# Performance work log

Measured on AMD Instinct MI355X. Metric: run time of the kernel, lower is better.

## Reference

```python
import jax, jax.numpy as jnp
import numpy as np

B, T, D = 4096, 200, 64
H1, H2 = 128, 64


def setup_inputs() -> dict:
    key = jax.random.key(0)
    ks = jax.random.split(key, 9)
    def glorot(k, shape):
        fan_in, fan_out = shape[0], shape[1]
        lim = float(np.sqrt(6.0 / (fan_in + fan_out)))
        return jax.random.uniform(k, shape, jnp.float32, -lim, lim)
    return {
        "candidate_embedding": jax.random.normal(ks[0], (B, D), jnp.float32),
        "history_embeddings": jax.random.normal(ks[1], (B, T, D), jnp.float32),
        "mask": jax.random.randint(ks[2], (B, T), 0, 2, jnp.int32),
        "W1": glorot(ks[3], (4 * D, H1)),
        "b1": jnp.zeros((H1,), jnp.float32),
        "W2": glorot(ks[4], (H1, H2)),
        "b2": jnp.zeros((H2,), jnp.float32),
        "W3": glorot(ks[5], (H2, 1)),
        "b3": jnp.zeros((1,), jnp.float32),
    }


def reference(candidate_embedding, history_embeddings, mask, W1, b1, W2, b2, W3, b3):
    # candidate: [B, D] -> broadcast to [B, T, D]
    cand = candidate_embedding[:, None, :]  # [B, 1, D]
    cand = jnp.broadcast_to(cand, history_embeddings.shape)
    # DIN feature concat: [B, T, 4D]
    feats = jnp.concatenate(
        [cand, history_embeddings, cand - history_embeddings, cand * history_embeddings],
        axis=-1,
    )
    # small MLP scorer per position
    h = jax.nn.relu(jnp.einsum("btf,fh->bth", feats, W1) + b1)
    h = jax.nn.relu(jnp.einsum("btf,fh->bth", h, W2) + b2)
    scores = (jnp.einsum("btf,fo->bto", h, W3) + b3)[..., 0]  # [B, T]
    # masked softmax over T
    scores = jnp.where(mask == 0, jnp.float32(-1e9), scores)
    weights = jax.nn.softmax(scores, axis=1)  # [B, T]
    # weighted sum over history: [B, D]
    return jnp.einsum("btd,bt->bd", history_embeddings, weights)
```

## Files before the change

### kernel.cpp

```cpp
#include <hip/hip_runtime.h>
#include <hip/hip_bf16.h>

#define NB 4096
#define NT 200
#define ND 64
#define NH1 128
#define NH2 64

#define WS_WX 0
#define WS_WC 16384
#define WS_W2 24576
#define WS_B1 32768
#define WS_B2 32896
#define WS_W3 32960
#define WS_B3 33024

__device__ __align__(16) float  g_wxt[8192];
__device__ __align__(16) float  g_wdt[8192];
__device__ __align__(16) __bf16 g_w2ts[8192];
__device__ __align__(16) __bf16 g_w2tsh[8192];
__device__ __align__(16) __bf16 g_w2tsl[8192];

typedef __bf16 bf16x8 __attribute__((ext_vector_type(8)));
typedef __bf16 bf16x4 __attribute__((ext_vector_type(4)));
typedef float  f32x4  __attribute__((ext_vector_type(4)));

__device__ __forceinline__ float ldany(const void* p, int i, int bf) {
    if (bf) return __bfloat162float(((const __hip_bfloat16*)p)[i]);
    return ((const float*)p)[i];
}

__global__ __launch_bounds__(256) void prep_kernel(
    const void* W1, const void* b1, const void* W2, const void* b2,
    const void* W3, const void* b3, int* flag_out, float* F) {
    __shared__ int votes;
    int tid = threadIdx.x;
    if (tid == 0) votes = 0;
    __syncthreads();
    {
        const unsigned* w1u = (const unsigned*)W1;
        unsigned w = w1u[tid];
        unsigned lo = w & 0xFFFFu;
        unsigned e = (lo >> 7) & 0xFFu;
        if (lo == 0u || (e >= 96u && e <= 124u)) atomicAdd(&votes, 1);
    }
    __syncthreads();
    int bf = (votes >= 160) ? 1 : 0;
    if (blockIdx.x == 0 && tid == 0) flag_out[0] = bf;

    int gtid = blockIdx.x * blockDim.x + tid;
    int gstride = gridDim.x * blockDim.x;

    for (int e = gtid; e < 8192; e += gstride) {
        int k = e >> 7, j = e & 127;
        float w1b = ldany(W1, (64 + k) * 128 + j, bf);
        float w1c = ldany(W1, (128 + k) * 128 + j, bf);
        float w1a = ldany(W1, k * 128 + j, bf);
        float w1d = ldany(W1, (192 + k) * 128 + j, bf);
        float wx = w1b - w1c;
        F[WS_WX + e] = wx;
        F[WS_WX + 8192 + e] = w1d;
        F[WS_WC + e] = w1a + w1c;
        g_wxt[j * 64 + k] = wx;
        g_wdt[j * 64 + k] = w1d;
        float w2v = ldany(W2, e, bf);
        F[WS_W2 + e] = w2v;
        int j2 = e & 63, k2 = e >> 6;
        int so = j2 * 128 + (k2 ^ ((j2 & 15) << 3));
        g_w2ts[so] = (__bf16)w2v;
        __bf16 w2h = (__bf16)w2v;
        g_w2tsh[so] = w2h;
        g_w2tsl[so] = (__bf16)(w2v - (float)w2h);
    }
    for (int e = gtid; e < 128; e += gstride) F[WS_B1 + e] = ldany(b1, e, bf);
    for (int e = gtid; e < 64; e += gstride) {
        F[WS_B2 + e] = ldany(b2, e, bf);
        F[WS_W3 + e] = ldany(W3, e, bf);
    }
    if (gtid == 0) F[WS_B3] = ldany(b3, 0, bf);
}

__device__ __forceinline__ void compute_chunk(
    int w, int lane, int tbase, int b, const int* mask,
    const __bf16* sH, const __bf16* sWhi, const __bf16* sWlo,
    const __bf16* sW2, __bf16* h1hi, __bf16* h1lo,
    const float* cbias, const float* b2s, const float* W3s, float b3v,
    float* ss)
{
    const int lq = lane >> 4, lr = lane & 15;
    const int t0 = 16 * w;

    const int ar = t0 + lr;
    const int asw = (ar & 7) << 3;
    const bf16x8 a0 = *(const bf16x8*)&sH[ar * 64 + ((lq * 8) ^ asw)];
    const bf16x8 a1 = *(const bf16x8*)&sH[ar * 64 + ((32 + lq * 8) ^ asw)];

#pragma unroll
    for (int n = 0; n < 8; n++) {
        const int col = n * 16 + lr;
        const int bsw = (col & 7) << 3;
        const int wb = col * 64;
        const float cb = cbias[col];
        f32x4 c = {cb, cb, cb, cb};
        c = __builtin_amdgcn_mfma_f32_16x16x32_bf16(
                a0, *(const bf16x8*)&sWhi[wb + ((lq * 8) ^ bsw)], c, 0, 0, 0);
        c = __builtin_amdgcn_mfma_f32_16x16x32_bf16(
                a1, *(const bf16x8*)&sWhi[wb + ((32 + lq * 8) ^ bsw)], c, 0, 0, 0);
        c = __builtin_amdgcn_mfma_f32_16x16x32_bf16(
                a0, *(const bf16x8*)&sWlo[wb + ((lq * 8) ^ bsw)], c, 0, 0, 0);
        c = __builtin_amdgcn_mfma_f32_16x16x32_bf16(
                a1, *(const bf16x8*)&sWlo[wb + ((32 + lq * 8) ^ bsw)], c, 0, 0, 0);
#pragma unroll
        for (int r = 0; r < 4; r++) {
            const int row = lq * 4 + r;
            const int hoff = row * 128 + (col ^ ((row & 15) << 3));
            float v = fmaxf(c[r], 0.f);
            __bf16 hi = (__bf16)v;
            h1hi[hoff] = hi;
            h1lo[hoff] = (__bf16)(v - (float)hi);
        }
    }

    f32x4 acc2[4];
#pragma unroll
    for (int n = 0; n < 4; n++) {
        const float bb = b2s[n * 16 + lr];
        acc2[n] = (f32x4){bb, bb, bb, bb};
    }
    const int a2sw = lr << 3;
#pragma unroll
    for (int s = 0; s < 4; s++) {
        const int k0 = s * 32 + lq * 8;
        const bf16x8 ah = *(const bf16x8*)&h1hi[lr * 128 + (k0 ^ a2sw)];
        const bf16x8 al = *(const bf16x8*)&h1lo[lr * 128 + (k0 ^ a2sw)];
#pragma unroll
        for (int n = 0; n < 4; n++) {
            const int col = n * 16 + lr;
            const bf16x8 bb =
                *(const bf16x8*)&sW2[col * 128 + (k0 ^ ((col & 15) << 3))];
            acc2[n] = __builtin_amdgcn_mfma_f32_16x16x32_bf16(ah, bb, acc2[n], 0, 0, 0);
            acc2[n] = __builtin_amdgcn_mfma_f32_16x16x32_bf16(al, bb, acc2[n], 0, 0, 0);
        }
    }

#pragma unroll
    for (int r = 0; r < 4; r++) {
        float p = 0.f;
#pragma unroll
        for (int n = 0; n < 4; n++)
            p = fmaf(fmaxf(acc2[n][r], 0.f), W3s[n * 16 + lr], p);
        p += __shfl_xor(p, 1);
        p += __shfl_xor(p, 2);
        p += __shfl_xor(p, 4);
        p += __shfl_xor(p, 8);
        const int gt = tbase + t0 + lq * 4 + r;
        if (lr == 0 && gt < NT)
            ss[gt] = (mask[(long)b * NT + gt] != 0) ? (p + b3v) : -1e9f;
    }
}

__global__ __launch_bounds__(512) void attn_bf16_kernel(
    const void* cand, const void* hist, const int* mask,
    const int* flag_p, const float* F, void* out)
{
    if (flag_p[0] == 0) return;

    __shared__ __align__(16) __bf16 sWhi[8192];
    __shared__ __align__(16) __bf16 sWlo[8192];
    __shared__ __align__(16) __bf16 sW2[8192];
    __shared__ __align__(16) __bf16 sH[8192];
    __shared__ __align__(16) __bf16 sH1[32768];
    __shared__ float cbias[128];
    __shared__ float cs[64], W3s[64], b2s[64];
    __shared__ float ss[NT];
    __shared__ float sred[8];
    __shared__ float part[8 * 65];
    __shared__ float b3s;

    const int tid = threadIdx.x;
    const int b = blockIdx.x;
    const int w = tid >> 6, lane = tid & 63;
    const __hip_bfloat16* hp = (const __hip_bfloat16*)hist;

    if (tid < 64) {
        cs[tid] = __bfloat162float(((const __hip_bfloat16*)cand)[(long)b * 64 + tid]);
        W3s[tid] = F[WS_W3 + tid];
        b2s[tid] = F[WS_B2 + tid];
    }
    if (tid == 0) b3s = F[WS_B3];
    *(uint4*)((char*)sW2 + tid * 16) =
        *(const uint4*)((const char*)g_w2ts + tid * 16);
    *(uint4*)((char*)sW2 + 8192 + tid * 16) =
        *(const uint4*)((const char*)g_w2ts + 8192 + tid * 16);
#pragma unroll
    for (int i = 0; i < 2; i++) {
        const int idx = tid + i * 512;
        const int t = idx >> 3, q = idx & 7;
        uint4 v = *(const uint4*)(hp + ((long)b * NT + t) * 64 + q * 8);
        *(uint4*)&sH[t * 64 + ((q * 8) ^ ((t & 7) << 3))] = v;
    }
    __syncthreads();

#pragma unroll
    for (int i = 0; i < 16; i++) {
        const int e = tid + i * 512;
        const int j = e >> 6, k = e & 63;
        float wv = fmaf(cs[k], g_wdt[e], g_wxt[e]);
        __bf16 hi = (__bf16)wv;
        const int off = j * 64 + (k ^ ((j & 7) << 3));
        sWhi[off] = hi;
        sWlo[off] = (__bf16)(wv - (float)hi);
    }
    {
        const int j = tid >> 2, kq = (tid & 3) << 4;
        float a = 0.f;
#pragma unroll
        for (int k2 = 0; k2 < 16; k2++)
            a = fmaf(cs[kq + k2], F[WS_WC + (kq + k2) * 128 + j], a);
        a += __shfl_xor(a, 1);
        a += __shfl_xor(a, 2);
        if ((tid & 3) == 0) cbias[j] = a + F[WS_B1 + j];
    }
    uint4 c1a, c1b = {0, 0, 0, 0};
    {
        const int t = 128 + (tid >> 3), q = tid & 7;
        c1a = *(const uint4*)(hp + ((long)b * NT + t) * 64 + q * 8);
    }
    if (tid < 64) {
        const int t = 192 + (tid >> 3), q = tid & 7;
        c1b = *(const uint4*)(hp + ((long)b * NT + t) * 64 + q * 8);
    }
    __builtin_amdgcn_sched_barrier(0);
    __syncthreads();

    const float b3v = b3s;
    compute_chunk(w, lane, 0, b, mask, sH, sWhi, sWlo, sW2,
                  &sH1[w * 4096], &sH1[w * 4096 + 2048],
                  cbias, b2s, W3s, b3v, ss);
    __syncthreads();

    {
        const int t = tid >> 3, q = tid & 7;
        *(uint4*)&sH[t * 64 + ((q * 8) ^ ((t & 7) << 3))] = c1a;
    }
    if (tid < 64) {
        const int t = 64 + (tid >> 3), q = tid & 7;
        *(uint4*)&sH[t * 64 + ((q * 8) ^ ((t & 7) << 3))] = c1b;
    }
    if (tid < 64) {
        const int t = 72 + (tid >> 3), q = tid & 7;
        uint4 z = {0, 0, 0, 0};
        *(uint4*)&sH[t * 64 + ((q * 8) ^ ((t & 7) << 3))] = z;
    }
    __syncthreads();

    if (w < 5)
        compute_chunk(w, lane, 128, b, mask, sH, sWhi, sWlo, sW2,
                      &sH1[w * 4096], &sH1[w * 4096 + 2048],
                      cbias, b2s, W3s, b3v, ss);
    __syncthreads();

    float v = (tid < NT) ? ss[tid] : -3.0e38f;
    if (tid < 256) {
        float m = v;
#pragma unroll
        for (int o = 32; o; o >>= 1) m = fmaxf(m, __shfl_xor(m, o));
        if ((tid & 63) == 0) sred[tid >> 6] = m;
    }
    __syncthreads();
    const float M = fmaxf(fmaxf(sred[0], sred[1]), fmaxf(sred[2], sred[3]));
    float p = (tid < NT) ? __expf(v - M) : 0.f;
    if (tid < 256) {
        float s2 = p;
#pragma unroll
        for (int o = 32; o; o >>= 1) s2 += __shfl_xor(s2, o);
        if ((tid & 63) == 0) sred[4 + (tid >> 6)] = s2;
    }
    __syncthreads();
    const float S = sred[4] + sred[5] + sred[6] + sred[7];
    if (tid < NT) ss[tid] = p / S;
    __syncthreads();

    const int d = tid & 63, g = tid >> 6;
    float acc = 0.f;
    for (int t = g; t < NT; t += 8)
        acc = fmaf(ss[t], __bfloat162float(hp[((long)b * NT + t) * 64 + d]), acc);
    part[g * 65 + d] = acc;
    __syncthreads();
    if (tid < 64) {
        float o = 0.f;
#pragma unroll
        for (int g2 = 0; g2 < 8; g2++) o += part[g2 * 65 + tid];
        ((__hip_bfloat16*)out)[b * 64 + tid] = __float2bfloat16(o);
    }
}

__device__ __forceinline__ void compute_chunk_f32(
    int w, int lane, int tbase, int b, const int* mask,
    const __bf16* sHhi, const __bf16* sHlo,
    const __bf16* sWhi, const __bf16* sWlo,
    const __bf16* sW2h, const __bf16* sW2l,
    __bf16* h1hi, __bf16* h1lo,
    const float* cbias, const float* b2s, const float* W3s, float b3v,
    float* ss)
{
    const int lq = lane >> 4, lr = lane & 15;
    const int t0 = 16 * w;

    const int ar = t0 + lr;
    const int asw = (ar & 7) << 3;
    const bf16x8 a0h = *(const bf16x8*)&sHhi[ar * 64 + ((lq * 8) ^ asw)];
    const bf16x8 a1h = *(const bf16x8*)&sHhi[ar * 64 + ((32 + lq * 8) ^ asw)];
    const bf16x8 a0l = *(const bf16x8*)&sHlo[ar * 64 + ((lq * 8) ^ asw)];
    const bf16x8 a1l = *(const bf16x8*)&sHlo[ar * 64 + ((32 + lq * 8) ^ asw)];
    __syncthreads();

#pragma unroll
    for (int n = 0; n < 8; n++) {
        const int col = n * 16 + lr;
        const int bsw = (col & 7) << 3;
        const int wb = col * 64;
        const float cb = cbias[col];
        f32x4 c = {cb, cb, cb, cb};
        const bf16x8 bh0 = *(const bf16x8*)&sWhi[wb + ((lq * 8) ^ bsw)];
        const bf16x8 bh1 = *(const bf16x8*)&sWhi[wb + ((32 + lq * 8) ^ bsw)];
        const bf16x8 bl0 = *(const bf16x8*)&sWlo[wb + ((lq * 8) ^ bsw)];
        const bf16x8 bl1 = *(const bf16x8*)&sWlo[wb + ((32 + lq * 8) ^ bsw)];
        c = __builtin_amdgcn_mfma_f32_16x16x32_bf16(a0h, bh0, c, 0, 0, 0);
        c = __builtin_amdgcn_mfma_f32_16x16x32_bf16(a1h, bh1, c, 0, 0, 0);
        c = __builtin_amdgcn_mfma_f32_16x16x32_bf16(a0l, bh0, c, 0, 0, 0);
        c = __builtin_amdgcn_mfma_f32_16x16x32_bf16(a1l, bh1, c, 0, 0, 0);
        c = __builtin_amdgcn_mfma_f32_16x16x32_bf16(a0h, bl0, c, 0, 0, 0);
        c = __builtin_amdgcn_mfma_f32_16x16x32_bf16(a1h, bl1, c, 0, 0, 0);
#pragma unroll
        for (int r = 0; r < 4; r++) {
            const int row = lq * 4 + r;
            const int hoff = row * 128 + (col ^ ((row & 15) << 3));
            float v = fmaxf(c[r], 0.f);
            __bf16 hi = (__bf16)v;
            h1hi[hoff] = hi;
            h1lo[hoff] = (__bf16)(v - (float)hi);
        }
    }

    f32x4 acc2[4];
#pragma unroll
    for (int n = 0; n < 4; n++) {
        const float bb = b2s[n * 16 + lr];
        acc2[n] = (f32x4){bb, bb, bb, bb};
    }
    const int a2sw = lr << 3;
#pragma unroll
    for (int s = 0; s < 4; s++) {
        const int k0 = s * 32 + lq * 8;
        const bf16x8 ah = *(const bf16x8*)&h1hi[lr * 128 + (k0 ^ a2sw)];
        const bf16x8 al = *(const bf16x8*)&h1lo[lr * 128 + (k0 ^ a2sw)];
#pragma unroll
        for (int n = 0; n < 4; n++) {
            const int col = n * 16 + lr;
            const int csw = (col & 15) << 3;
            const bf16x8 bh = *(const bf16x8*)&sW2h[col * 128 + (k0 ^ csw)];
            const bf16x8 bl = *(const bf16x8*)&sW2l[col * 128 + (k0 ^ csw)];
            acc2[n] = __builtin_amdgcn_mfma_f32_16x16x32_bf16(ah, bh, acc2[n], 0, 0, 0);
            acc2[n] = __builtin_amdgcn_mfma_f32_16x16x32_bf16(al, bh, acc2[n], 0, 0, 0);
            acc2[n] = __builtin_amdgcn_mfma_f32_16x16x32_bf16(ah, bl, acc2[n], 0, 0, 0);
        }
    }

#pragma unroll
    for (int r = 0; r < 4; r++) {
        float p = 0.f;
#pragma unroll
        for (int n = 0; n < 4; n++)
            p = fmaf(fmaxf(acc2[n][r], 0.f), W3s[n * 16 + lr], p);
        p += __shfl_xor(p, 1);
        p += __shfl_xor(p, 2);
        p += __shfl_xor(p, 4);
        p += __shfl_xor(p, 8);
        const int gt = tbase + t0 + lq * 4 + r;
        if (lr == 0 && gt < NT)
            ss[gt] = (mask[(long)b * NT + gt] != 0) ? (p + b3v) : -1e9f;
    }
}

__global__ __launch_bounds__(512) void attn_f32_kernel(
    const void* cand, const void* hist, const int* mask,
    const int* flag_p, const float* F, void* out)
{
    if (flag_p[0] != 0) return;

    __shared__ __align__(16) __bf16 sWhi[8192];
    __shared__ __align__(16) __bf16 sWlo[8192];
    __shared__ __align__(16) __bf16 sW2h[8192];
    __shared__ __align__(16) __bf16 sW2l[8192];
    __shared__ __align__(16) __bf16 uBuf[32768];
    __shared__ float cbias[128];
    __shared__ float cs[64], W3s[64], b2s[64];
    __shared__ float ss[NT];
    __shared__ float sred[8];
    __shared__ float b3s;

    const int tid = threadIdx.x;
    const int b = blockIdx.x;
    const int w = tid >> 6, lane = tid & 63;
    const float* hf = (const float*)hist;

    __bf16* sHhi = uBuf;
    __bf16* sHlo = uBuf + 8192;
    __bf16* h1hi = uBuf + w * 4096;
    __bf16* h1lo = uBuf + w * 4096 + 2048;

    if (tid < 64) {
        cs[tid] = ((const float*)cand)[(long)b * 64 + tid];
        W3s[tid] = F[WS_W3 + tid];
        b2s[tid] = F[WS_B2 + tid];
    }
    if (tid == 0) b3s = F[WS_B3];
#pragma unroll
    for (int i = 0; i < 2; i++) {
        const int off = (tid + i * 512) * 16;
        *(uint4*)((char*)sW2h + off) = *(const uint4*)((const char*)g_w2tsh + off);
        *(uint4*)((char*)sW2l + off) = *(const uint4*)((const char*)g_w2tsl + off);
    }
#pragma unroll
    for (int i = 0; i < 4; i++) {
        const int e4 = tid + i * 512;
        const int t = e4 >> 4, k = (e4 & 15) * 4;
        float4 v = *(const float4*)&hf[((long)b * NT + t) * 64 + k];
        bf16x4 hi4, lo4;
        hi4[0] = (__bf16)v.x; lo4[0] = (__bf16)(v.x - (float)hi4[0]);
        hi4[1] = (__bf16)v.y; lo4[1] = (__bf16)(v.y - (float)hi4[1]);
        hi4[2] = (__bf16)v.z; lo4[2] = (__bf16)(v.z - (float)hi4[2]);
        hi4[3] = (__bf16)v.w; lo4[3] = (__bf16)(v.w - (float)hi4[3]);
        const int pos = ((k & 56) ^ ((t & 7) << 3)) | (k & 4);
        *(bf16x4*)&sHhi[t * 64 + pos] = hi4;
        *(bf16x4*)&sHlo[t * 64 + pos] = lo4;
    }
    __syncthreads();

#pragma unroll
    for (int i = 0; i < 16; i++) {
        const int e = tid + i * 512;
        const int j = e >> 6, k = e & 63;
        float wv = fmaf(cs[k], g_wdt[e], g_wxt[e]);
        __bf16 hi = (__bf16)wv;
        const int off = j * 64 + (k ^ ((j & 7) << 3));
        sWhi[off] = hi;
        sWlo[off] = (__bf16)(wv - (float)hi);
    }
    {
        const int j = tid >> 2, kq = (tid & 3) << 4;
        float a = 0.f;
#pragma unroll
        for (int k2 = 0; k2 < 16; k2++)
            a = fmaf(cs[kq + k2], F[WS_WC + (kq + k2) * 128 + j], a);
        a += __shfl_xor(a, 1);
        a += __shfl_xor(a, 2);
        if ((tid & 3) == 0) cbias[j] = a + F[WS_B1 + j];
    }
    float4 c1a0, c1a1, c1b = {0.f, 0.f, 0.f, 0.f};
    {
        int e4 = tid;
        int tl = e4 >> 4, k = (e4 & 15) * 4;
        c1a0 = *(const float4*)&hf[((long)b * NT + 128 + tl) * 64 + k];
        e4 = tid + 512;
        tl = e4 >> 4; k = (e4 & 15) * 4;
        c1a1 = *(const float4*)&hf[((long)b * NT + 128 + tl) * 64 + k];
    }
    if (tid < 128) {
        const int e4 = 1024 + tid;
        const int tl = e4 >> 4, k = (e4 & 15) * 4;
        c1b = *(const float4*)&hf[((long)b * NT + 128 + tl) * 64 + k];
    }
    __builtin_amdgcn_sched_barrier(0);
    __syncthreads();

    const float b3v = b3s;
    compute_chunk_f32(w, lane, 0, b, mask, sHhi, sHlo, sWhi, sWlo, sW2h, sW2l,
                      h1hi, h1lo, cbias, b2s, W3s, b3v, ss);
    __syncthreads();

    {
        int e4 = tid;
        int tl = e4 >> 4, k = (e4 & 15) * 4;
        int pos = ((k & 56) ^ ((tl & 7) << 3)) | (k & 4);
        bf16x4 hi4, lo4;
        hi4[0] = (__bf16)c1a0.x; lo4[0] = (__bf16)(c1a0.x - (float)hi4[0]);
        hi4[1] = (__bf16)c1a0.y; lo4[1] = (__bf16)(c1a0.y - (float)hi4[1]);
        hi4[2] = (__bf16)c1a0.z; lo4[2] = (__bf16)(c1a0.z - (float)hi4[2]);
        hi4[3] = (__bf16)c1a0.w; lo4[3] = (__bf16)(c1a0.w - (float)hi4[3]);
        *(bf16x4*)&sHhi[tl * 64 + pos] = hi4;
        *(bf16x4*)&sHlo[tl * 64 + pos] = lo4;
        e4 = tid + 512;
        tl = e4 >> 4; k = (e4 & 15) * 4;
        pos = ((k & 56) ^ ((tl & 7) << 3)) | (k & 4);
        hi4[0] = (__bf16)c1a1.x; lo4[0] = (__bf16)(c1a1.x - (float)hi4[0]);
        hi4[1] = (__bf16)c1a1.y; lo4[1] = (__bf16)(c1a1.y - (float)hi4[1]);
        hi4[2] = (__bf16)c1a1.z; lo4[2] = (__bf16)(c1a1.z - (float)hi4[2]);
        hi4[3] = (__bf16)c1a1.w; lo4[3] = (__bf16)(c1a1.w - (float)hi4[3]);
        *(bf16x4*)&sHhi[tl * 64 + pos] = hi4;
        *(bf16x4*)&sHlo[tl * 64 + pos] = lo4;
    }
    if (tid < 128) {
        const int e4 = 1024 + tid;
        const int tl = e4 >> 4, k = (e4 & 15) * 4;
        const int pos = ((k & 56) ^ ((tl & 7) << 3)) | (k & 4);
        bf16x4 hi4, lo4;
        hi4[0] = (__bf16)c1b.x; lo4[0] = (__bf16)(c1b.x - (float)hi4[0]);
        hi4[1] = (__bf16)c1b.y; lo4[1] = (__bf16)(c1b.y - (float)hi4[1]);
        hi4[2] = (__bf16)c1b.z; lo4[2] = (__bf16)(c1b.z - (float)hi4[2]);
        hi4[3] = (__bf16)c1b.w; lo4[3] = (__bf16)(c1b.w - (float)hi4[3]);
        *(bf16x4*)&sHhi[tl * 64 + pos] = hi4;
        *(bf16x4*)&sHlo[tl * 64 + pos] = lo4;
    }
    if (tid < 128) {
        const int tl = 72 + (tid >> 4), k = (tid & 15) * 4;
        const int pos = ((k & 56) ^ ((tl & 7) << 3)) | (k & 4);
        bf16x4 z;
        z[0] = (__bf16)0.f; z[1] = (__bf16)0.f; z[2] = (__bf16)0.f; z[3] = (__bf16)0.f;
        *(bf16x4*)&sHhi[tl * 64 + pos] = z;
        *(bf16x4*)&sHlo[tl * 64 + pos] = z;
    }
    __syncthreads();

    compute_chunk_f32(w, lane, 128, b, mask, sHhi, sHlo, sWhi, sWlo, sW2h, sW2l,
                      h1hi, h1lo, cbias, b2s, W3s, b3v, ss);
    __syncthreads();

    float v = (tid < NT) ? ss[tid] : -3.0e38f;
    if (tid < 256) {
        float m = v;
#pragma unroll
        for (int o = 32; o; o >>= 1) m = fmaxf(m, __shfl_xor(m, o));
        if ((tid & 63) == 0) sred[tid >> 6] = m;
    }
    __syncthreads();
    const float M = fmaxf(fmaxf(sred[0], sred[1]), fmaxf(sred[2], sred[3]));
    float p = (tid < NT) ? __expf(v - M) : 0.f;
    if (tid < 256) {
        float s2 = p;
#pragma unroll
        for (int o = 32; o; o >>= 1) s2 += __shfl_xor(s2, o);
        if ((tid & 63) == 0) sred[4 + (tid >> 6)] = s2;
    }
    __syncthreads();
    const float S = sred[4] + sred[5] + sred[6] + sred[7];
    if (tid < NT) ss[tid] = p / S;
    __syncthreads();

    float* part = (float*)uBuf;
    const int d = tid & 63, g = tid >> 6;
    float acc = 0.f;
    for (int t = g; t < NT; t += 8)
        acc = fmaf(ss[t], hf[((long)b * NT + t) * 64 + d], acc);
    part[g * 65 + d] = acc;
    __syncthreads();
    if (tid < 64) {
        float o = 0.f;
#pragma unroll
        for (int g2 = 0; g2 < 8; g2++) o += part[g2 * 65 + tid];
        ((float*)out)[b * 64 + tid] = o;
    }
}

extern "C" void kernel_launch(void* const* d_in, const int* in_sizes, int n_in,
                              void* d_out, int out_size, void* d_ws, size_t ws_size,
                              hipStream_t stream) {
    const void* cand = d_in[0];
    const void* hist = d_in[1];
    const int* mask = (const int*)d_in[2];
    const void* W1 = d_in[3];
    const void* b1 = d_in[4];
    const void* W2 = d_in[5];
    const void* b2 = d_in[6];
    const void* W3 = d_in[7];
    const void* b3 = d_in[8];

    int* flag = (int*)d_ws;
    float* F = (float*)((char*)d_ws + 256);

    prep_kernel<<<32, 256, 0, stream>>>(W1, b1, W2, b2, W3, b3, flag, F);
    attn_f32_kernel<<<NB, 512, 0, stream>>>(cand, hist, mask, flag, F, d_out);
    attn_bf16_kernel<<<NB, 512, 0, stream>>>(cand, hist, mask, flag, F, d_out);
}
```

Before: 506.7 us.

## Shrink LDS footprint by splitting layer-1 into halves and reading W2 from global

The layer-1 output is now computed in two 64-column halves, staged in a shared buffer aliased with the history tile, and consumed by layer 2 between block barriers. W2 is read directly from global/L2 instead of being copied into LDS. The partial-sum buffer also reuses the same memory, and launch bounds request 4 waves per SIMD. The W1 combine loop is vectorised with float4 loads and bf16x4 stores. The intent is to cut LDS use so more blocks fit per CU. The cost is extra __syncthreads inside the compute chunk and global-memory latency on W2 reads. In the bf16 path all 8 waves now run the second chunk instead of only 5.

Result: slower. 611.0 us (+20.6%).

```diff
diff --git a/kernel.cpp b/kernel.cpp
--- a/kernel.cpp
+++ b/kernel.cpp
@@ -80,46 +80,20 @@
     if (gtid == 0) F[WS_B3] = ldany(b3, 0, bf);
 }
 
-__device__ __forceinline__ void compute_chunk(
+__device__ __forceinline__ void compute_chunk_bf(
     int w, int lane, int tbase, int b, const int* mask,
     const __bf16* sH, const __bf16* sWhi, const __bf16* sWlo,
-    const __bf16* sW2, __bf16* h1hi, __bf16* h1lo,
+    __bf16* h1hi, __bf16* h1lo,
     const float* cbias, const float* b2s, const float* W3s, float b3v,
     float* ss)
 {
     const int lq = lane >> 4, lr = lane & 15;
     const int t0 = 16 * w;
-
     const int ar = t0 + lr;
     const int asw = (ar & 7) << 3;
     const bf16x8 a0 = *(const bf16x8*)&sH[ar * 64 + ((lq * 8) ^ asw)];
     const bf16x8 a1 = *(const bf16x8*)&sH[ar * 64 + ((32 + lq * 8) ^ asw)];
-
-#pragma unroll
-    for (int n = 0; n < 8; n++) {
-        const int col = n * 16 + lr;
-        const int bsw = (col & 7) << 3;
-        const int wb = col * 64;
-        const float cb = cbias[col];
-        f32x4 c = {cb, cb, cb, cb};
-        c = __builtin_amdgcn_mfma_f32_16x16x32_bf16(
-                a0, *(const bf16x8*)&sWhi[wb + ((lq * 8) ^ bsw)], c, 0, 0, 0);
-        c = __builtin_amdgcn_mfma_f32_16x16x32_bf16(
-                a1, *(const bf16x8*)&sWhi[wb + ((32 + lq * 8) ^ bsw)], c, 0, 0, 0);
-        c = __builtin_amdgcn_mfma_f32_16x16x32_bf16(
-                a0, *(const bf16x8*)&sWlo[wb + ((lq * 8) ^ bsw)], c, 0, 0, 0);
-        c = __builtin_amdgcn_mfma_f32_16x16x32_bf16(
-                a1, *(const bf16x8*)&sWlo[wb + ((32 + lq * 8) ^ bsw)], c, 0, 0, 0);
-#pragma unroll
-        for (int r = 0; r < 4; r++) {
-            const int row = lq * 4 + r;
-            const int hoff = row * 128 + (col ^ ((row & 15) << 3));
-            float v = fmaxf(c[r], 0.f);
-            __bf16 hi = (__bf16)v;
-            h1hi[hoff] = hi;
-            h1lo[hoff] = (__bf16)(v - (float)hi);
-        }
-    }
+    __syncthreads();
 
     f32x4 acc2[4];
 #pragma unroll
@@ -127,20 +101,53 @@
         const float bb = b2s[n * 16 + lr];
         acc2[n] = (f32x4){bb, bb, bb, bb};
     }
-    const int a2sw = lr << 3;
-#pragma unroll
-    for (int s = 0; s < 4; s++) {
-        const int k0 = s * 32 + lq * 8;
-        const bf16x8 ah = *(const bf16x8*)&h1hi[lr * 128 + (k0 ^ a2sw)];
-        const bf16x8 al = *(const bf16x8*)&h1lo[lr * 128 + (k0 ^ a2sw)];
+
+#pragma unroll
+    for (int half = 0; half < 2; half++) {
 #pragma unroll
         for (int n = 0; n < 4; n++) {
-            const int col = n * 16 + lr;
-            const bf16x8 bb =
-                *(const bf16x8*)&sW2[col * 128 + (k0 ^ ((col & 15) << 3))];
-            acc2[n] = __builtin_amdgcn_mfma_f32_16x16x32_bf16(ah, bb, acc2[n], 0, 0, 0);
-            acc2[n] = __builtin_amdgcn_mfma_f32_16x16x32_bf16(al, bb, acc2[n], 0, 0, 0);
+            const int col = half * 64 + n * 16 + lr;
+            const int bsw = (col & 7) << 3;
+            const int wb = col * 64;
+            const float cb = cbias[col];
+            f32x4 c = {cb, cb, cb, cb};
+            const bf16x8 bh0 = *(const bf16x8*)&sWhi[wb + ((lq * 8) ^ bsw)];
+            const bf16x8 bh1 = *(const bf16x8*)&sWhi[wb + ((32 + lq * 8) ^ bsw)];
+            const bf16x8 bl0 = *(const bf16x8*)&sWlo[wb + ((lq * 8) ^ bsw)];
+            const bf16x8 bl1 = *(const bf16x8*)&sWlo[wb + ((32 + lq * 8) ^ bsw)];
+            c = __builtin_amdgcn_mfma_f32_16x16x32_bf16(a0, bh0, c, 0, 0, 0);
+            c = __builtin_amdgcn_mfma_f32_16x16x32_bf16(a1, bh1, c, 0, 0, 0);
+            c = __builtin_amdgcn_mfma_f32_16x16x32_bf16(a0, bl0, c, 0, 0, 0);
+            c = __builtin_amdgcn_mfma_f32_16x16x32_bf16(a1, bl1, c, 0, 0, 0);
+#pragma unroll
+            for (int r = 0; r < 4; r++) {
+                const int row = t0 + lq * 4 + r;
+                const int lcol = n * 16 + lr;
+                const int hoff = row * 64 + (lcol ^ ((row & 7) << 3));
+                float v = fmaxf(c[r], 0.f);
+                __bf16 hi = (__bf16)v;
+                h1hi[hoff] = hi;
+                h1lo[hoff] = (__bf16)(v - (float)hi);
+            }
         }
+        __syncthreads();
+#pragma unroll
+        for (int s = 0; s < 2; s++) {
+            const int kl = s * 32 + lq * 8;
+            const int kg = half * 64 + kl;
+            const int hoff2 = (t0 + lr) * 64 + (kl ^ ((lr & 7) << 3));
+            const bf16x8 ah = *(const bf16x8*)&h1hi[hoff2];
+            const bf16x8 al = *(const bf16x8*)&h1lo[hoff2];
+#pragma unroll
+            for (int n = 0; n < 4; n++) {
+                const int col = n * 16 + lr;
+                const int gso = col * 128 + (kg ^ ((col & 15) << 3));
+                const bf16x8 bb = *(const bf16x8*)&g_w2ts[gso];
+                acc2[n] = __builtin_amdgcn_mfma_f32_16x16x32_bf16(ah, bb, acc2[n], 0, 0, 0);
+                acc2[n] = __builtin_amdgcn_mfma_f32_16x16x32_bf16(al, bb, acc2[n], 0, 0, 0);
+            }
+        }
+        if (half == 0) __syncthreads();
     }
 
 #pragma unroll
@@ -159,7 +166,7 @@
     }
 }
 
-__global__ __launch_bounds__(512) void attn_bf16_kernel(
+__global__ __launch_bounds__(512, 4) void attn_bf16_kernel(
     const void* cand, const void* hist, const int* mask,
     const int* flag_p, const float* F, void* out)
 {
@@ -167,14 +174,11 @@
 
     __shared__ __align__(16) __bf16 sWhi[8192];
     __shared__ __align__(16) __bf16 sWlo[8192];
-    __shared__ __align__(16) __bf16 sW2[8192];
-    __shared__ __align__(16) __bf16 sH[8192];
-    __shared__ __align__(16) __bf16 sH1[32768];
+    __shared__ __align__(16) __bf16 uBuf[16384];
     __shared__ float cbias[128];
     __shared__ float cs[64], W3s[64], b2s[64];
     __shared__ float ss[NT];
     __shared__ float sred[8];
-    __shared__ float part[8 * 65];
     __shared__ float b3s;
 
     const int tid = threadIdx.x;
@@ -182,16 +186,16 @@
     const int w = tid >> 6, lane = tid & 63;
     const __hip_bfloat16* hp = (const __hip_bfloat16*)hist;
 
+    __bf16* sH = uBuf;
+    __bf16* h1hi = uBuf;
+    __bf16* h1lo = uBuf + 8192;
+
     if (tid < 64) {
         cs[tid] = __bfloat162float(((const __hip_bfloat16*)cand)[(long)b * 64 + tid]);
         W3s[tid] = F[WS_W3 + tid];
         b2s[tid] = F[WS_B2 + tid];
     }
     if (tid == 0) b3s = F[WS_B3];
-    *(uint4*)((char*)sW2 + tid * 16) =
-        *(const uint4*)((const char*)g_w2ts + tid * 16);
-    *(uint4*)((char*)sW2 + 8192 + tid * 16) =
-        *(const uint4*)((const char*)g_w2ts + 8192 + tid * 16);
 #pragma unroll
     for (int i = 0; i < 2; i++) {
         const int idx = tid + i * 512;
@@ -202,14 +206,23 @@
     __syncthreads();
 
 #pragma unroll
-    for (int i = 0; i < 16; i++) {
-        const int e = tid + i * 512;
-        const int j = e >> 6, k = e & 63;
-        float wv = fmaf(cs[k], g_wdt[e], g_wxt[e]);
-        __bf16 hi = (__bf16)wv;
-        const int off = j * 64 + (k ^ ((j & 7) << 3));
-        sWhi[off] = hi;
-        sWlo[off] = (__bf16)(wv - (float)hi);
+    for (int i = 0; i < 4; i++) {
+        const int e4 = tid + i * 512;
+        const int j = e4 >> 4, k4 = (e4 & 15) << 2;
+        const float4 wx = *(const float4*)&g_wxt[e4 * 4];
+        const float4 wd = *(const float4*)&g_wdt[e4 * 4];
+        bf16x4 hi4, lo4;
+        float v0 = fmaf(cs[k4 + 0], wd.x, wx.x);
+        float v1 = fmaf(cs[k4 + 1], wd.y, wx.y);
+        float v2 = fmaf(cs[k4 + 2], wd.z, wx.z);
+        float v3 = fmaf(cs[k4 + 3], wd.w, wx.w);
+        hi4[0] = (__bf16)v0; lo4[0] = (__bf16)(v0 - (float)hi4[0]);
+        hi4[1] = (__bf16)v1; lo4[1] = (__bf16)(v1 - (float)hi4[1]);
+        hi4[2] = (__bf16)v2; lo4[2] = (__bf16)(v2 - (float)hi4[2]);
+        hi4[3] = (__bf16)v3; lo4[3] = (__bf16)(v3 - (float)hi4[3]);
+        const int off = j * 64 + (k4 ^ ((j & 7) << 3));
+        *(bf16x4*)&sWhi[off] = hi4;
+        *(bf16x4*)&sWlo[off] = lo4;
     }
     {
         const int j = tid >> 2, kq = (tid & 3) << 4;
@@ -234,9 +247,8 @@
     __syncthreads();
 
     const float b3v = b3s;
-    compute_chunk(w, lane, 0, b, mask, sH, sWhi, sWlo, sW2,
-                  &sH1[w * 4096], &sH1[w * 4096 + 2048],
-                  cbias, b2s, W3s, b3v, ss);
+    compute_chunk_bf(w, lane, 0, b, mask, sH, sWhi, sWlo, h1hi, h1lo,
+                     cbias, b2s, W3s, b3v, ss);
     __syncthreads();
 
     {
@@ -254,10 +266,8 @@
     }
     __syncthreads();
 
-    if (w < 5)
-        compute_chunk(w, lane, 128, b, mask, sH, sWhi, sWlo, sW2,
-                      &sH1[w * 4096], &sH1[w * 4096 + 2048],
-                      cbias, b2s, W3s, b3v, ss);
+    compute_chunk_bf(w, lane, 128, b, mask, sH, sWhi, sWlo, h1hi, h1lo,
+                     cbias, b2s, W3s, b3v, ss);
     __syncthreads();
 
     float v = (tid < NT) ? ss[tid] : -3.0e38f;
@@ -281,6 +291,7 @@
     if (tid < NT) ss[tid] = p / S;
     __syncthreads();
 
+    float* part = (float*)uBuf;
     const int d = tid & 63, g = tid >> 6;
     float acc = 0.f;
     for (int t = g; t < NT; t += 8)
@@ -299,14 +310,12 @@
     int w, int lane, int tbase, int b, const int* mask,
     const __bf16* sHhi, const __bf16* sHlo,
     const __bf16* sWhi, const __bf16* sWlo,
-    const __bf16* sW2h, const __bf16* sW2l,
     __bf16* h1hi, __bf16* h1lo,
     const float* cbias, const float* b2s, const float* W3s, float b3v,
     float* ss)
 {
     const int lq = lane >> 4, lr = lane & 15;
     const int t0 = 16 * w;
-
     const int ar = t0 + lr;
     const int asw = (ar & 7) << 3;
     const bf16x8 a0h = *(const bf16x8*)&sHhi[ar * 64 + ((lq * 8) ^ asw)];
@@ -315,56 +324,63 @@
     const bf16x8 a1l = *(const bf16x8*)&sHlo[ar * 64 + ((32 + lq * 8) ^ asw)];
     __syncthreads();
 
-#pragma unroll
-    for (int n = 0; n < 8; n++) {
-        const int col = n * 16 + lr;
-        const int bsw = (col & 7) << 3;
-        const int wb = col * 64;
-        const float cb = cbias[col];
-        f32x4 c = {cb, cb, cb, cb};
-        const bf16x8 bh0 = *(const bf16x8*)&sWhi[wb + ((lq * 8) ^ bsw)];
-        const bf16x8 bh1 = *(const bf16x8*)&sWhi[wb + ((32 + lq * 8) ^ bsw)];
-        const bf16x8 bl0 = *(const bf16x8*)&sWlo[wb + ((lq * 8) ^ bsw)];
-        const bf16x8 bl1 = *(const bf16x8*)&sWlo[wb + ((32 + lq * 8) ^ bsw)];
-        c = __builtin_amdgcn_mfma_f32_16x16x32_bf16(a0h, bh0, c, 0, 0, 0);
-        c = __builtin_amdgcn_mfma_f32_16x16x32_bf16(a1h, bh1, c, 0, 0, 0);
-        c = __builtin_amdgcn_mfma_f32_16x16x32_bf16(a0l, bh0, c, 0, 0, 0);
-        c = __builtin_amdgcn_mfma_f32_16x16x32_bf16(a1l, bh1, c, 0, 0, 0);
-        c = __builtin_amdgcn_mfma_f32_16x16x32_bf16(a0h, bl0, c, 0, 0, 0);
-        c = __builtin_amdgcn_mfma_f32_16x16x32_bf16(a1h, bl1, c, 0, 0, 0);
-#pragma unroll
-        for (int r = 0; r < 4; r++) {
-            const int row = lq * 4 + r;
-            const int hoff = row * 128 + (col ^ ((row & 15) << 3));
-            float v = fmaxf(c[r], 0.f);
-            __bf16 hi = (__bf16)v;
-            h1hi[hoff] = hi;
-            h1lo[hoff] = (__bf16)(v - (float)hi);
-        }
-    }
-
     f32x4 acc2[4];
 #pragma unroll
     for (int n = 0; n < 4; n++) {
         const float bb = b2s[n * 16 + lr];
         acc2[n] = (f32x4){bb, bb, bb, bb};
     }
-    const int a2sw = lr << 3;
-#pragma unroll
-    for (int s = 0; s < 4; s++) {
-        const int k0 = s * 32 + lq * 8;
-        const bf16x8 ah = *(const bf16x8*)&h1hi[lr * 128 + (k0 ^ a2sw)];
-        const bf16x8 al = *(const bf16x8*)&h1lo[lr * 128 + (k0 ^ a2sw)];
+
+#pragma unroll
+    for (int half = 0; half < 2; half++) {
 #pragma unroll
         for (int n = 0; n < 4; n++) {
-            const int col = n * 16 + lr;
-            const int csw = (col & 15) << 3;
-            const bf16x8 bh = *(const bf16x8*)&sW2h[col * 128 + (k0 ^ csw)];
-            const bf16x8 bl = *(const bf16x8*)&sW2l[col * 128 + (k0 ^ csw)];
-            acc2[n] = __builtin_amdgcn_mfma_f32_16x16x32_bf16(ah, bh, acc2[n], 0, 0, 0);
-            acc2[n] = __builtin_amdgcn_mfma_f32_16x16x32_bf16(al, bh, acc2[n], 0, 0, 0);
-            acc2[n] = __builtin_amdgcn_mfma_f32_16x16x32_bf16(ah, bl, acc2[n], 0, 0, 0);
+            const int col = half * 64 + n * 16 + lr;
+            const int bsw = (col & 7) << 3;
+            const int wb = col * 64;
+            const float cb = cbias[col];
+            f32x4 c = {cb, cb, cb, cb};
+            const bf16x8 bh0 = *(const bf16x8*)&sWhi[wb + ((lq * 8) ^ bsw)];
+            const bf16x8 bh1 = *(const bf16x8*)&sWhi[wb + ((32 + lq * 8) ^ bsw)];
+            const bf16x8 bl0 = *(const bf16x8*)&sWlo[wb + ((lq * 8) ^ bsw)];
+            const bf16x8 bl1 = *(const bf16x8*)&sWlo[wb + ((32 + lq * 8) ^ bsw)];
+            c = __builtin_amdgcn_mfma_f32_16x16x32_bf16(a0h, bh0, c, 0, 0, 0);
+            c = __builtin_amdgcn_mfma_f32_16x16x32_bf16(a1h, bh1, c, 0, 0, 0);
+            c = __builtin_amdgcn_mfma_f32_16x16x32_bf16(a0l, bh0, c, 0, 0, 0);
+            c = __builtin_amdgcn_mfma_f32_16x16x32_bf16(a1l, bh1, c, 0, 0, 0);
+            c = __builtin_amdgcn_mfma_f32_16x16x32_bf16(a0h, bl0, c, 0, 0, 0);
+            c = __builtin_amdgcn_mfma_f32_16x16x32_bf16(a1h, bl1, c, 0, 0, 0);
+#pragma unroll
+            for (int r = 0; r < 4; r++) {
+                const int row = t0 + lq * 4 + r;
+                const int lcol = n * 16 + lr;
+                const int hoff = row * 64 + (lcol ^ ((row & 7) << 3));
+                float v = fmaxf(c[r], 0.f);
+                __bf16 hi = (__bf16)v;
+                h1hi[hoff] = hi;
+                h1lo[hoff] = (__bf16)(v - (float)hi);
+            }
         }
+        __syncthreads();
+#pragma unroll
+        for (int s = 0; s < 2; s++) {
+            const int kl = s * 32 + lq * 8;
+            const int kg = half * 64 + kl;
+            const int hoff2 = (t0 + lr) * 64 + (kl ^ ((lr & 7) << 3));
+            const bf16x8 ah = *(const bf16x8*)&h1hi[hoff2];
+            const bf16x8 al = *(const bf16x8*)&h1lo[hoff2];
+#pragma unroll
+            for (int n = 0; n < 4; n++) {
+                const int col = n * 16 + lr;
+                const int gso = col * 128 + (kg ^ ((col & 15) << 3));
+                const bf16x8 bh = *(const bf16x8*)&g_w2tsh[gso];
+                const bf16x8 bl = *(const bf16x8*)&g_w2tsl[gso];
+                acc2[n] = __builtin_amdgcn_mfma_f32_16x16x32_bf16(ah, bh, acc2[n], 0, 0, 0);
+                acc2[n] = __builtin_amdgcn_mfma_f32_16x16x32_bf16(al, bh, acc2[n], 0, 0, 0);
+                acc2[n] = __builtin_amdgcn_mfma_f32_16x16x32_bf16(ah, bl, acc2[n], 0, 0, 0);
+            }
+        }
+        if (half == 0) __syncthreads();
     }
 
 #pragma unroll
@@ -383,7 +399,7 @@
     }
 }
 
-__global__ __launch_bounds__(512) void attn_f32_kernel(
+__global__ __launch_bounds__(512, 4) void attn_f32_kernel(
     const void* cand, const void* hist, const int* mask,
     const int* flag_p, const float* F, void* out)
 {
@@ -391,9 +407,7 @@
 
     __shared__ __align__(16) __bf16 sWhi[8192];
     __shared__ __align__(16) __bf16 sWlo[8192];
-    __shared__ __align__(16) __bf16 sW2h[8192];
-    __shared__ __align__(16) __bf16 sW2l[8192];
-    __shared__ __align__(16) __bf16 uBuf[32768];
+    __shared__ __align__(16) __bf16 uBuf[16384];
     __shared__ float cbias[128];
     __shared__ float cs[64], W3s[64], b2s[64];
     __shared__ float ss[NT];
@@ -407,8 +421,8 @@
 
     __bf16* sHhi = uBuf;
     __bf16* sHlo = uBuf + 8192;
-    __bf16* h1hi = uBuf + w * 4096;
-    __bf16* h1lo = uBuf + w * 4096 + 2048;
+    __bf16* h1hi = uBuf;
+    __bf16* h1lo = uBuf + 8192;
 
     if (tid < 64) {
         cs[tid] = ((const float*)cand)[(long)b * 64 + tid];
@@ -416,12 +430,6 @@
         b2s[tid] = F[WS_B2 + tid];
     }
     if (tid == 0) b3s = F[WS_B3];
-#pragma unroll
-    for (int i = 0; i < 2; i++) {
-        const int off = (tid + i * 512) * 16;
-        *(uint4*)((char*)sW2h + off) = *(const uint4*)((const char*)g_w2tsh + off);
-        *(uint4*)((char*)sW2l + off) = *(const uint4*)((const char*)g_w2tsl + off);
-    }
 #pragma unroll
     for (int i = 0; i < 4; i++) {
         const int e4 = tid + i * 512;
@@ -439,14 +447,23 @@
     __syncthreads();
 
 #pragma unroll
-    for (int i = 0; i < 16; i++) {
-        const int e = tid + i * 512;
-        const int j = e >> 6, k = e & 63;
-        float wv = fmaf(cs[k], g_wdt[e], g_wxt[e]);
-        __bf16 hi = (__bf16)wv;
-        const int off = j * 64 + (k ^ ((j & 7) << 3));
-        sWhi[off] = hi;
-        sWlo[off] = (__bf16)(wv - (float)hi);
+    for (int i = 0; i < 4; i++) {
+        const int e4 = tid + i * 512;
+        const int j = e4 >> 4, k4 = (e4 & 15) << 2;
+        const float4 wx = *(const float4*)&g_wxt[e4 * 4];
+        const float4 wd = *(const float4*)&g_wdt[e4 * 4];
+        bf16x4 hi4, lo4;
+        float v0 = fmaf(cs[k4 + 0], wd.x, wx.x);
+        float v1 = fmaf(cs[k4 + 1], wd.y, wx.y);
+        float v2 = fmaf(cs[k4 + 2], wd.z, wx.z);
+        float v3 = fmaf(cs[k4 + 3], wd.w, wx.w);
+        hi4[0] = (__bf16)v0; lo4[0] = (__bf16)(v0 - (float)hi4[0]);
+        hi4[1] = (__bf16)v1; lo4[1] = (__bf16)(v1 - (float)hi4[1]);
+        hi4[2] = (__bf16)v2; lo4[2] = (__bf16)(v2 - (float)hi4[2]);
+        hi4[3] = (__bf16)v3; lo4[3] = (__bf16)(v3 - (float)hi4[3]);
+        const int off = j * 64 + (k4 ^ ((j & 7) << 3));
+        *(bf16x4*)&sWhi[off] = hi4;
+        *(bf16x4*)&sWlo[off] = lo4;
     }
     {
         const int j = tid >> 2, kq = (tid & 3) << 4;
@@ -476,7 +493,7 @@
     __syncthreads();
 
     const float b3v = b3s;
-    compute_chunk_f32(w, lane, 0, b, mask, sHhi, sHlo, sWhi, sWlo, sW2h, sW2l,
+    compute_chunk_f32(w, lane, 0, b, mask, sHhi, sHlo, sWhi, sWlo,
                       h1hi, h1lo, cbias, b2s, W3s, b3v, ss);
     __syncthreads();
 
@@ -523,7 +540,7 @@
     }
     __syncthreads();
 
-    compute_chunk_f32(w, lane, 128, b, mask, sHhi, sHlo, sWhi, sWlo, sW2h, sW2l,
+    compute_chunk_f32(w, lane, 128, b, mask, sHhi, sHlo, sWhi, sWlo,
                       h1hi, h1lo, cbias, b2s, W3s, b3v, ss);
     __syncthreads();
 
```
